# Performance work log

Hardware: AMD Instinct MI355X
Metric: run time of the kernel (lower is better)

Reference implementation:

```python
import jax, jax.numpy as jnp
import numpy as np

N, E, F, H, C = 100000, 1600000, 128, 128, 16
NEG_SLOPE = 0.01  # torch F.leaky_relu default


def setup_inputs() -> dict:
    key = jax.random.key(0)
    ks = jax.random.split(key, 32)
    inp = {
        "x": jax.random.normal(ks[0], (N, F), jnp.float32),
        "edge_index": jax.random.randint(ks[1], (2, E), 0, N, jnp.int32),
        "edge_weight": jax.random.uniform(ks[2], (E,), jnp.float32),
    }
    def w(k, fan_in, fan_out):
        s = 1.0 / np.sqrt(fan_in)
        return jax.random.uniform(k, (fan_in, fan_out), jnp.float32, -s, s)
    # cell 0: pre 128->128, arma 128->128, sage 128->128
    inp["pre_w0"] = w(ks[3], F, H); inp["pre_b0"] = jnp.zeros((H,), jnp.float32)
    inp["arma_w0"] = w(ks[4], H, H); inp["arma_v0"] = w(ks[5], H, H); inp["arma_b0"] = jnp.zeros((H,), jnp.float32)
    inp["sage_wl0"] = w(ks[6], H, H); inp["sage_bl0"] = jnp.zeros((H,), jnp.float32); inp["sage_wr0"] = w(ks[7], H, H)
    # cell 1: pre 256->128 (cell0 outputs 2H)
    inp["pre_w1"] = w(ks[8], 2 * H, H); inp["pre_b1"] = jnp.zeros((H,), jnp.float32)
    inp["arma_w1"] = w(ks[9], H, H); inp["arma_v1"] = w(ks[10], H, H); inp["arma_b1"] = jnp.zeros((H,), jnp.float32)
    inp["sage_wl1"] = w(ks[11], H, H); inp["sage_bl1"] = jnp.zeros((H,), jnp.float32); inp["sage_wr1"] = w(ks[12], H, H)
    inp["cls_w"] = w(ks[13], 2 * H, C); inp["cls_b"] = jnp.zeros((C,), jnp.float32)
    return inp


def _cell(h, row, col, norm, ew, cnt, n, arma_w, arma_v, arma_b, sage_wl, sage_bl, sage_wr):
    # ARMAConv (num_stacks=1, num_layers=1): relu(A_hat (h W) + h V + b), A_hat = sym-norm adj (no self loops)
    t = h @ arma_w
    agg = jax.ops.segment_sum(norm[:, None] * t[row], col, num_segments=n)
    h1 = jax.nn.leaky_relu(jax.nn.relu(agg + h @ arma_v + arma_b), NEG_SLOPE)
    # SAGEConv (mean aggr of edge-weighted messages): lin_l(mean_j w_ij h_j) + lin_r(h_i)
    s = jax.ops.segment_sum(ew[:, None] * h[row], col, num_segments=n)
    h2 = jax.nn.leaky_relu((s / cnt[:, None]) @ sage_wl + sage_bl + h @ sage_wr, NEG_SLOPE)
    return jax.nn.elu(jnp.concatenate([h1, h2], axis=1))


def reference(x, edge_index, edge_weight,
              pre_w0, pre_b0, arma_w0, arma_v0, arma_b0, sage_wl0, sage_bl0, sage_wr0,
              pre_w1, pre_b1, arma_w1, arma_v1, arma_b1, sage_wl1, sage_bl1, sage_wr1,
              cls_w, cls_b):
    n = x.shape[0]
    row, col = edge_index[0], edge_index[1]  # messages flow row -> col
    # gcn_norm without self loops (ARMAConv)
    deg = jax.ops.segment_sum(edge_weight, col, num_segments=n)
    dinv = jnp.where(deg > 0, 1.0 / jnp.sqrt(jnp.where(deg > 0, deg, 1.0)), 0.0)
    norm = dinv[row] * edge_weight * dinv[col]
    # scatter_mean denominator (edge counts, clamped to 1)
    cnt = jnp.maximum(jax.ops.segment_sum(jnp.ones_like(edge_weight), col, num_segments=n), 1.0)
    h = x  # eval mode: input dropout is identity
    for p in [(pre_w0, pre_b0, arma_w0, arma_v0, arma_b0, sage_wl0, sage_bl0, sage_wr0),
              (pre_w1, pre_b1, arma_w1, arma_v1, arma_b1, sage_wl1, sage_bl1, sage_wr1)]:
        pw, pb = p[0], p[1]
        h = _cell(h @ pw + pb, row, col, norm, edge_weight, cnt, n, *p[2:])
    logits = h @ cls_w + cls_b
    return jax.nn.log_softmax(logits, axis=-1)
```

## Files before the change

kernel.cpp:

```cpp
#include <hip/hip_runtime.h>
#include <hip/hip_bf16.h>
#include <hip/hip_fp16.h>

typedef __bf16 bf16x8 __attribute__((ext_vector_type(8)));
typedef float f32x4 __attribute__((ext_vector_type(4)));
typedef unsigned short ushort_t;
typedef unsigned int uint_t;

#if defined(__has_builtin)
#if __has_builtin(__builtin_amdgcn_global_load_lds)
#define HAS_GLL 1
#endif
#endif

__device__ inline float blo(uint_t v) { return __uint_as_float(v << 16); }
__device__ inline float bhi(uint_t v) { return __uint_as_float(v & 0xffff0000u); }
__device__ inline ushort_t f2b(float f) {
  uint_t u = __float_as_uint(f);
  uint_t r = (u + 0x7fffu + ((u >> 16) & 1u)) >> 16;
  return (ushort_t)r;
}
__device__ inline uint_t pk2(float a, float b) {
  return (uint_t)f2b(a) | ((uint_t)f2b(b) << 16);
}


__global__ __launch_bounds__(256) void bcount_k(const int* __restrict__ col,
                                                int* __restrict__ bcnt, int E, int NB) {
  __shared__ int h[256];
  int t = threadIdx.x;
  h[t] = 0;
  __syncthreads();
  int e0 = blockIdx.x * 8192;
#pragma unroll
  for (int j = 0; j < 32; ++j) {
    int e = e0 + j * 256 + t;
    if (e < E) atomicAdd(&h[col[e] >> 9], 1);
  }
  __syncthreads();
  if (t < NB && h[t] > 0) atomicAdd(&bcnt[t], h[t]);
}

__global__ __launch_bounds__(256) void bscan_k(const int* __restrict__ bcnt,
                                               int* __restrict__ bbase, int* __restrict__ cursor,
                                               int* __restrict__ offs, int NB, int N, int E) {
  __shared__ int sd[256];
  int t = threadIdx.x;
  int v = (t < NB) ? bcnt[t] : 0;
  int acc = v;
  sd[t] = v; __syncthreads();
  for (int off = 1; off < 256; off <<= 1) {
    int x = (t >= off) ? sd[t - off] : 0;
    __syncthreads();
    acc += x; sd[t] = acc;
    __syncthreads();
  }
  if (t < NB) { bbase[t] = acc - v; cursor[t] = acc - v; }
  if (t == 0) { bbase[NB] = E; offs[N] = E; }
}

__global__ __launch_bounds__(512) void bscatter_k(
    const int* __restrict__ row, const int* __restrict__ col, const float* __restrict__ ew,
    int* __restrict__ cursor, uint2* __restrict__ eout, int E, int NB) {
  __shared__ int h[256];
  __shared__ int lofs[256];
  __shared__ int lcur[256];
  __shared__ int gbase[256];
  __shared__ int sc[256];
  __shared__ uint2 stage[8192];
  __shared__ int addr[8192];
  int t = threadIdx.x;
  int e0 = blockIdx.x * 8192;
  int cnt = min(8192, E - e0);
  if (t < 256) h[t] = 0;
  __syncthreads();
#pragma unroll
  for (int j = 0; j < 16; ++j) {
    int e = e0 + j * 512 + t;
    if (e < E) atomicAdd(&h[col[e] >> 9], 1);
  }
  __syncthreads();
  int s = (t < 256) ? h[t] : 0;
  int acc = s;
  if (t < 256) sc[t] = s;
  __syncthreads();
  for (int off = 1; off < 256; off <<= 1) {
    int x = (t < 256 && t >= off) ? sc[t - off] : 0;
    __syncthreads();
    if (t < 256) { acc += x; sc[t] = acc; }
    __syncthreads();
  }
  if (t < NB && s > 0) gbase[t] = atomicAdd(&cursor[t], s);
  if (t < 256) { lofs[t] = acc - s; lcur[t] = acc - s; }
  __syncthreads();
#pragma unroll
  for (int j = 0; j < 16; ++j) {
    int e = e0 + j * 512 + t;
    if (e < E) {
      int c = col[e];
      int bk = c >> 9;
      int p = atomicAdd(&lcur[bk], 1);
      uint2 v;
      v.x = ((uint_t)(c & 511) << 17) | (uint_t)row[e];
      v.y = __float_as_uint(ew[e]);
      stage[p] = v;
      addr[p] = gbase[bk] + (p - lofs[bk]);
    }
  }
  __syncthreads();
  for (int i = t; i < cnt; i += 512) eout[addr[i]] = stage[i];
}

__global__ __launch_bounds__(512) void bsort_k(
    const uint2* __restrict__ ein, const int* __restrict__ bbase,
    int* __restrict__ offs, float* __restrict__ dinv, float* __restrict__ cinv,
    uint2* __restrict__ eout, int N) {
  __shared__ int h[512];
  __shared__ int lcur[512];
  __shared__ float degs[512];
  __shared__ int sd[512];
  int t = threadIdx.x, b = blockIdx.x;
  int base = bbase[b], end = bbase[b + 1];
  int cnt = end - base;
  int node0 = b << 9;
  h[t] = 0;
  degs[t] = 0.f;
  __syncthreads();
  for (int i = t; i < cnt; i += 512) {
    uint2 v = ein[base + i];
    int lc = v.x >> 17;
    atomicAdd(&h[lc], 1);
    atomicAdd(&degs[lc], __uint_as_float(v.y));
  }
  __syncthreads();
  int s = h[t];
  int acc = s;
  sd[t] = s; __syncthreads();
  for (int off = 1; off < 512; off <<= 1) {
    int x = (t >= off) ? sd[t - off] : 0;
    __syncthreads();
    acc += x; sd[t] = acc;
    __syncthreads();
  }
  int excl = acc - s;
  lcur[t] = excl;
  int node = node0 + t;
  if (node < N) {
    offs[node] = base + excl;
    float d = degs[t];
    dinv[node] = d > 0.f ? rsqrtf(d) : 0.f;
    cinv[node] = 1.0f / fmaxf((float)s, 1.f);
  }
  __syncthreads();
  for (int i = t; i < cnt; i += 512) {
    uint2 v = ein[base + i];
    int lc = v.x >> 17;
    int p = atomicAdd(&lcur[lc], 1);
    uint2 o;
    o.x = v.x & 0x1FFFF;
    o.y = v.y;
    eout[base + p] = o;
  }
}

__global__ void edgew_k(uint2* __restrict__ sedge, const float* __restrict__ dinv, int E) {
  int e = blockIdx.x * blockDim.x + threadIdx.x;
  if (e < E) {
    uint2 v = sedge[e];
    float ew = __uint_as_float(v.y);
    float wA = dinv[v.x] * ew;
    uint_t lo = (uint_t)__half_as_ushort(__float2half_rn(wA));
    uint_t hi = (uint_t)__half_as_ushort(__float2half_rn(ew));
    sedge[e].y = lo | (hi << 16);
  }
}

struct WP { const float* p[12]; };
__global__ void wtp_k(WP wp, ushort_t* __restrict__ wt) {
  int b = blockIdx.x;
  int t = threadIdx.x;
  if (b < 11) {
    const float* W = wp.p[b];
    ushort_t* T = wt + (size_t)b * 128 * 128;
    for (int i = 0; i < 64; ++i) {
      int lin = i * 256 + t;
      int k = lin >> 7, c = lin & 127;
      T[c * 128 + k] = f2b(W[lin]);
    }
  } else {
    const float* W = wp.p[11];
    ushort_t* T = wt + (size_t)11 * 128 * 128;
    for (int i = 0; i < 16; ++i) {
      int lin = i * 256 + t;
      int c = lin >> 8, k = lin & 255;
      T[lin] = f2b(W[k * 16 + c]);
    }
  }
}

__global__ __launch_bounds__(256) void agg_k(
    const uint_t* __restrict__ hp2, const uint2* __restrict__ sedge,
    const float* __restrict__ dinv, const float* __restrict__ cinv,
    const int* __restrict__ offs,
    uint_t* __restrict__ outA, uint_t* __restrict__ outS, int n) {
  int wid = threadIdx.x >> 6;
  int lane = threadIdx.x & 63;
  int half = lane >> 5, li = lane & 31;
  int node = blockIdx.x * 4 + wid;
  if (node >= n) return;
  int s0 = __builtin_amdgcn_readfirstlane(offs[node]);
  int e0 = __builtin_amdgcn_readfirstlane(offs[node + 1]);
  const char* hpb = (const char*)hp2;
  uint_t libase = (uint_t)(li << 3);
  float a0 = 0.f, a1 = 0.f, a2 = 0.f, a3 = 0.f;
  float m0 = 0.f, m1 = 0.f, m2 = 0.f, m3 = 0.f;
  for (int p = s0; p < e0; p += 8) {
    uint2 ed[4];
#pragma unroll
    for (int j = 0; j < 4; ++j) {
      int k = p + 2 * j + half;
      ed[j] = sedge[k < e0 ? k : s0];
    }
#pragma unroll
    for (int j = 0; j < 4; ++j) {
      int k = p + 2 * j + half;
      bool ok = (k < e0);
      uint_t w = ok ? ed[j].y : 0u;
      uint2 v = *(const uint2*)(hpb + ((ed[j].x << 8) | libase));
      float wA = __half2float(__ushort_as_half((ushort_t)(w & 0xffff)));
      float wS = __half2float(__ushort_as_half((ushort_t)(w >> 16)));
      float f0 = blo(v.x), f1 = bhi(v.x), f2 = blo(v.y), f3 = bhi(v.y);
      a0 += wA * f0; a1 += wA * f1; a2 += wA * f2; a3 += wA * f3;
      m0 += wS * f0; m1 += wS * f1; m2 += wS * f2; m3 += wS * f3;
    }
  }
  a0 += __shfl_xor(a0, 32); a1 += __shfl_xor(a1, 32);
  a2 += __shfl_xor(a2, 32); a3 += __shfl_xor(a3, 32);
  m0 += __shfl_xor(m0, 32); m1 += __shfl_xor(m1, 32);
  m2 += __shfl_xor(m2, 32); m3 += __shfl_xor(m3, 32);
  if (half == 0) {
    float dn = dinv[node];
    uint2 o;
    o.x = pk2(dn * a0, dn * a1);
    o.y = pk2(dn * a2, dn * a3);
    *(uint2*)&outA[(size_t)node * 64 + li * 2] = o;
  } else {
    float cn = cinv[node];
    uint2 o;
    o.x = pk2(cn * m0, cn * m1);
    o.y = pk2(cn * m2, cn * m3);
    *(uint2*)&outS[(size_t)node * 64 + li * 2] = o;
  }
}

__device__ inline int swz(int r, int k) { return (r * 128 + k) ^ ((r & 7) << 3); }
__device__ inline int cswz(int r, int k) { return (r * 256 + k) ^ ((r & 7) << 3); }

__device__ inline void stage_tile(const ushort_t* __restrict__ A, ushort_t* lds,
                                  int rowBase, int wid, int lane) {
  int lr = lane >> 4, lchunk = lane & 15;
#ifdef HAS_GLL
#pragma unroll
  for (int i = 0; i < 8; ++i) {
    int r = wid * 32 + i * 4 + lr;
    int csrc = (lchunk ^ (r & 7)) << 4;
    const char* g = (const char*)A + (((size_t)(rowBase + r)) << 8) + csrc;
    char* l = (char*)lds + ((wid * 32 + i * 4) << 8);
    __builtin_amdgcn_global_load_lds((const __attribute__((address_space(1))) void*)g,
                                     (__attribute__((address_space(3))) void*)l, 16, 0, 0);
  }
#else
#pragma unroll
  for (int i = 0; i < 8; ++i) {
    int r = wid * 32 + i * 4 + lr;
    uint4 v = *(const uint4*)&A[((size_t)(rowBase + r)) * 128 + lchunk * 8];
    *(uint4*)&lds[swz(r, lchunk * 8)] = v;
  }
#endif
}

__device__ inline void stage_wait() {
#ifdef HAS_GLL
  asm volatile("s_waitcnt vmcnt(0)" ::: "memory");
#endif
}

__device__ inline bf16x8 ldw(const ushort_t* __restrict__ Wt, int wc, int nn, int k, int lane) {
  int c = wc * 64 + nn * 16 + (lane & 15);
  return *(const bf16x8*)&Wt[c * 128 + k * 32 + (lane >> 4) * 8];
}

__device__ inline bf16x8 lda(const ushort_t* lds, int wr, int m, int k, int lane) {
  return *(const bf16x8*)&lds[swz(wr * 64 + m * 16 + (lane & 15), k * 32 + (lane >> 4) * 8)];
}

template <int ACT>
__device__ inline void epilogue(f32x4 (&acc)[4][4], const float* __restrict__ bias,
                                ushort_t* __restrict__ out, int rowBase, int wr, int wc,
                                int lane, int nrows) {
#pragma unroll
  for (int m = 0; m < 4; ++m) {
    int gr0 = rowBase + wr * 64 + m * 16 + (lane >> 4) * 4;
#pragma unroll
    for (int nn = 0; nn < 4; ++nn) {
      int gc = wc * 64 + nn * 16 + (lane & 15);
      float bv = bias[gc];
#pragma unroll
      for (int j = 0; j < 4; ++j) {
        int gr = gr0 + j;
        if (gr < nrows) {
          float v = acc[m][nn][j] + bv;
          if (ACT == 1) v = fmaxf(v, 0.f);
          if (ACT == 2) v = v > 0.f ? v : (__expf(0.01f * v) - 1.f);
          out[(size_t)gr * 128 + gc] = f2b(v);
        }
      }
    }
  }
}

__global__ __launch_bounds__(256, 2) void pre0_k(
    const float* __restrict__ Xf, const ushort_t* __restrict__ Wt,
    const float* __restrict__ bias, ushort_t* __restrict__ out, int nrows) {
  __shared__ ushort_t As[128 * 128];
  int t = threadIdx.x, lane = t & 63, wid = t >> 6;
  int wr = wid >> 1, wc = wid & 1;
  int rowBase = blockIdx.x * 128;
#pragma unroll
  for (int i = 0; i < 16; ++i) {
    int f = t + i * 256;
    int r = f >> 5, q = f & 31;
    int gr = rowBase + r;
    float4 v = make_float4(0.f, 0.f, 0.f, 0.f);
    if (gr < nrows) v = *(const float4*)&Xf[(size_t)gr * 128 + q * 4];
    uint2 o;
    o.x = pk2(v.x, v.y);
    o.y = pk2(v.z, v.w);
    *(uint2*)&As[swz(r, q * 4)] = o;
  }
  __syncthreads();
  f32x4 acc[4][4] = {};
#pragma unroll
  for (int k = 0; k < 4; ++k) {
    bf16x8 af[4], wf[4];
#pragma unroll
    for (int m = 0; m < 4; ++m) af[m] = lda(As, wr, m, k, lane);
#pragma unroll
    for (int nn = 0; nn < 4; ++nn) wf[nn] = ldw(Wt, wc, nn, k, lane);
#pragma unroll
    for (int m = 0; m < 4; ++m)
#pragma unroll
      for (int nn = 0; nn < 4; ++nn)
        acc[m][nn] = __builtin_amdgcn_mfma_f32_16x16x32_bf16(af[m], wf[nn], acc[m][nn], 0, 0, 0);
  }
  epilogue<0>(acc, bias, out, rowBase, wr, wc, lane, nrows);
}

template <int TAIL>
__global__ __launch_bounds__(256, 2) void dualfused_k(
    const ushort_t* __restrict__ X, const ushort_t* __restrict__ Y,
    const ushort_t* __restrict__ H,
    const ushort_t* __restrict__ WX, const ushort_t* __restrict__ WXH,
    const ushort_t* __restrict__ WY, const ushort_t* __restrict__ WYH,
    const float* __restrict__ bX, const float* __restrict__ bY,
    const ushort_t* __restrict__ WZ1, const ushort_t* __restrict__ WZ2,
    const float* __restrict__ bZ,
    ushort_t* __restrict__ outH, float* __restrict__ outL, int nrows) {
  __shared__ ushort_t buf[2 * 128 * 128];
  ushort_t* Xs = buf;
  ushort_t* Hs = buf + 128 * 128;
  int t = threadIdx.x, lane = t & 63, wid = t >> 6;
  int wr = wid >> 1, wc = wid & 1;
  int rowBase = blockIdx.x * 128;

  stage_tile(X, Xs, rowBase, wid, lane);
  stage_tile(H, Hs, rowBase, wid, lane);
  stage_wait();
  __syncthreads();

  uint_t h1p[4][4][2];
  {
    f32x4 acc[4][4] = {};
#pragma unroll
    for (int k = 0; k < 4; ++k) {
      bf16x8 af[4], hf[4], wx[4], wh[4];
#pragma unroll
      for (int m = 0; m < 4; ++m) { af[m] = lda(Xs, wr, m, k, lane); hf[m] = lda(Hs, wr, m, k, lane); }
#pragma unroll
      for (int nn = 0; nn < 4; ++nn) { wx[nn] = ldw(WX, wc, nn, k, lane); wh[nn] = ldw(WXH, wc, nn, k, lane); }
#pragma unroll
      for (int m = 0; m < 4; ++m)
#pragma unroll
        for (int nn = 0; nn < 4; ++nn) {
          acc[m][nn] = __builtin_amdgcn_mfma_f32_16x16x32_bf16(af[m], wx[nn], acc[m][nn], 0, 0, 0);
          acc[m][nn] = __builtin_amdgcn_mfma_f32_16x16x32_bf16(hf[m], wh[nn], acc[m][nn], 0, 0, 0);
        }
    }
#pragma unroll
    for (int m = 0; m < 4; ++m)
#pragma unroll
      for (int nn = 0; nn < 4; ++nn) {
        float bv = bX[wc * 64 + nn * 16 + (lane & 15)];
        float v0 = fmaxf(acc[m][nn][0] + bv, 0.f);
        float v1 = fmaxf(acc[m][nn][1] + bv, 0.f);
        float v2 = fmaxf(acc[m][nn][2] + bv, 0.f);
        float v3 = fmaxf(acc[m][nn][3] + bv, 0.f);
        h1p[m][nn][0] = pk2(v0, v1);
        h1p[m][nn][1] = pk2(v2, v3);
      }
  }

  __syncthreads();
  stage_tile(Y, Xs, rowBase, wid, lane);
  stage_wait();
  __syncthreads();

  f32x4 acc2[4][4] = {};
#pragma unroll
  for (int k = 0; k < 4; ++k) {
    bf16x8 af[4], hf[4], wy[4], wh[4];
#pragma unroll
    for (int m = 0; m < 4; ++m) { af[m] = lda(Xs, wr, m, k, lane); hf[m] = lda(Hs, wr, m, k, lane); }
#pragma unroll
    for (int nn = 0; nn < 4; ++nn) { wy[nn] = ldw(WY, wc, nn, k, lane); wh[nn] = ldw(WYH, wc, nn, k, lane); }
#pragma unroll
    for (int m = 0; m < 4; ++m)
#pragma unroll
      for (int nn = 0; nn < 4; ++nn) {
        acc2[m][nn] = __builtin_amdgcn_mfma_f32_16x16x32_bf16(af[m], wy[nn], acc2[m][nn], 0, 0, 0);
        acc2[m][nn] = __builtin_amdgcn_mfma_f32_16x16x32_bf16(hf[m], wh[nn], acc2[m][nn], 0, 0, 0);
      }
  }

  __syncthreads();

#pragma unroll
  for (int m = 0; m < 4; ++m) {
    int r0 = wr * 64 + m * 16 + (lane >> 4) * 4;
#pragma unroll
    for (int nn = 0; nn < 4; ++nn) {
      int c = wc * 64 + nn * 16 + (lane & 15);
      float bv = bY[c];
#pragma unroll
      for (int j = 0; j < 4; ++j) {
        int r = r0 + j;
        ushort_t h1v = (ushort_t)((h1p[m][nn][j >> 1] >> ((j & 1) * 16)) & 0xffff);
        buf[cswz(r, c)] = h1v;
        float v = acc2[m][nn][j] + bv;
        v = v > 0.f ? v : (__expf(0.01f * v) - 1.f);
        buf[cswz(r, 128 + c)] = f2b(v);
      }
    }
  }
  __syncthreads();

  if (TAIL == 0) {
    f32x4 acc3[4][4] = {};
#pragma unroll
    for (int kk = 0; kk < 8; ++kk) {
      const ushort_t* WZ = (kk < 4) ? WZ1 : WZ2;
      int kl = kk & 3;
      bf16x8 af[4], wf[4];
#pragma unroll
      for (int m = 0; m < 4; ++m) {
        int r = wr * 64 + m * 16 + (lane & 15);
        af[m] = *(const bf16x8*)&buf[cswz(r, kk * 32 + (lane >> 4) * 8)];
      }
#pragma unroll
      for (int nn = 0; nn < 4; ++nn) wf[nn] = ldw(WZ, wc, nn, kl, lane);
#pragma unroll
      for (int m = 0; m < 4; ++m)
#pragma unroll
        for (int nn = 0; nn < 4; ++nn)
          acc3[m][nn] = __builtin_amdgcn_mfma_f32_16x16x32_bf16(af[m], wf[nn], acc3[m][nn], 0, 0, 0);
    }
    epilogue<0>(acc3, bZ, outH, rowBase, wr, wc, lane, nrows);
  } else {
    f32x4 accc[2] = {};
#pragma unroll
    for (int kk = 0; kk < 8; ++kk) {
      bf16x8 bfr = *(const bf16x8*)&WZ1[(lane & 15) * 256 + kk * 32 + (lane >> 4) * 8];
#pragma unroll
      for (int mm = 0; mm < 2; ++mm) {
        int r = wid * 32 + mm * 16 + (lane & 15);
        bf16x8 af = *(const bf16x8*)&buf[cswz(r, kk * 32 + (lane >> 4) * 8)];
        accc[mm] = __builtin_amdgcn_mfma_f32_16x16x32_bf16(af, bfr, accc[mm], 0, 0, 0);
      }
    }
    float bc = bZ[lane & 15];
#pragma unroll
    for (int mm = 0; mm < 2; ++mm) {
#pragma unroll
      for (int j = 0; j < 4; ++j) {
        float lg = accc[mm][j] + bc;
        float mx = lg;
        for (int d = 1; d < 16; d <<= 1) mx = fmaxf(mx, __shfl_xor(mx, d));
        float ex = __expf(lg - mx);
        float sum = ex;
        for (int d = 1; d < 16; d <<= 1) sum += __shfl_xor(sum, d);
        float r_ = (lg - mx) - logf(sum);
        int grow = rowBase + wid * 32 + mm * 16 + (lane >> 4) * 4 + j;
        if (grow < nrows) outL[grow * 16 + (lane & 15)] = r_;
      }
    }
  }
}


extern "C" void kernel_launch(void* const* d_in, const int* in_sizes, int n_in,
                              void* d_out, int out_size, void* d_ws, size_t ws_size,
                              hipStream_t stream) {
  const float* x        = (const float*)d_in[0];
  const int*   eidx     = (const int*)d_in[1];
  const float* ew       = (const float*)d_in[2];
  const float* pre_w0   = (const float*)d_in[3];
  const float* pre_b0   = (const float*)d_in[4];
  const float* arma_w0  = (const float*)d_in[5];
  const float* arma_v0  = (const float*)d_in[6];
  const float* arma_b0  = (const float*)d_in[7];
  const float* sage_wl0 = (const float*)d_in[8];
  const float* sage_bl0 = (const float*)d_in[9];
  const float* sage_wr0 = (const float*)d_in[10];
  const float* pre_w1   = (const float*)d_in[11];
  const float* pre_b1   = (const float*)d_in[12];
  const float* arma_w1  = (const float*)d_in[13];
  const float* arma_v1  = (const float*)d_in[14];
  const float* arma_b1  = (const float*)d_in[15];
  const float* sage_wl1 = (const float*)d_in[16];
  const float* sage_bl1 = (const float*)d_in[17];
  const float* sage_wr1 = (const float*)d_in[18];
  const float* cls_w    = (const float*)d_in[19];
  const float* cls_b    = (const float*)d_in[20];

  const int N = in_sizes[0] / 128;
  const int E = in_sizes[2];
  const int N_pad = ((N + 127) / 128) * 128;
  const int NB = (N + 511) >> 9;
  const int* row = eidx;
  const int* col = eidx + E;

  char* p = (char*)d_ws;
  auto carve = [&](size_t bytes) { char* q = p; p += (bytes + 255) & ~(size_t)255; return q; };
  ushort_t* hp    = (ushort_t*)carve((size_t)N_pad * 128 * 2);
  ushort_t* bufA  = (ushort_t*)carve((size_t)N_pad * 128 * 2);
  ushort_t* bufS  = (ushort_t*)carve((size_t)N_pad * 128 * 2);
  ushort_t* wt    = (ushort_t*)carve(((size_t)11 * 128 * 128 + 16 * 256) * 2);
  uint2*  sedge  = (uint2*)carve((size_t)E * 8);
  uint2*  sedgeT = (uint2*)carve((size_t)E * 8);
  float*  dinv  = (float*)carve((size_t)N * 4);
  float*  cinv  = (float*)carve((size_t)N * 4);
  int*    offs  = (int*)carve((size_t)(N + 1) * 4);
  int*    bcnt  = (int*)carve((size_t)256 * 4);
  int*    bbase = (int*)carve((size_t)257 * 4);
  int*    cursor= (int*)carve((size_t)256 * 4);

  hipMemsetAsync(bcnt, 0, (size_t)256 * 4, stream);

  const int gE = (E + 8191) / 8192;
  bcount_k<<<gE, 256, 0, stream>>>(col, bcnt, E, NB);
  bscan_k<<<1, 256, 0, stream>>>(bcnt, bbase, cursor, offs, NB, N, E);
  bscatter_k<<<gE, 512, 0, stream>>>(row, col, ew, cursor, sedgeT, E, NB);
  bsort_k<<<NB, 512, 0, stream>>>(sedgeT, bbase, offs, dinv, cinv, sedge, N);
  edgew_k<<<(E + 255) / 256, 256, 0, stream>>>(sedge, dinv, E);

  WP wp;
  wp.p[0] = pre_w0;  wp.p[1] = arma_w0; wp.p[2] = arma_v0;
  wp.p[3] = sage_wl0; wp.p[4] = sage_wr0;
  wp.p[5] = pre_w1;  wp.p[6] = pre_w1 + 128 * 128;
  wp.p[7] = arma_w1; wp.p[8] = arma_v1;
  wp.p[9] = sage_wl1; wp.p[10] = sage_wr1;
  wp.p[11] = cls_w;
  wtp_k<<<12, 256, 0, stream>>>(wp, wt);

  const int gB = (N + 127) / 128;
  const int gA = (N + 3) / 4;
  auto WT = [&](int i) { return wt + (size_t)i * 128 * 128; };

  pre0_k<<<gB, 256, 0, stream>>>(x, WT(0), pre_b0, hp, N);
  agg_k<<<gA, 256, 0, stream>>>((const uint_t*)hp, sedge, dinv, cinv, offs,
                                (uint_t*)bufA, (uint_t*)bufS, N);
  dualfused_k<0><<<gB, 256, 0, stream>>>(bufA, bufS, hp, WT(1), WT(2), WT(3), WT(4),
                                         arma_b0, sage_bl0, WT(5), WT(6), pre_b1,
                                         hp, nullptr, N);
  agg_k<<<gA, 256, 0, stream>>>((const uint_t*)hp, sedge, dinv, cinv, offs,
                                (uint_t*)bufA, (uint_t*)bufS, N);
  dualfused_k<1><<<gB, 256, 0, stream>>>(bufA, bufS, hp, WT(7), WT(8), WT(9), WT(10),
                                         arma_b1, sage_bl1, WT(11), nullptr, cls_b,
                                         nullptr, (float*)d_out, N);
}
```

Before: 371.1 us.

## Retile dual fused GEMM kernel to 64-row blocks and stage X/Y/H together

The dual fused kernel now handles 64 rows per block instead of 128, with each wave owning a 32-column slice. The X, Y and H tiles are staged into shared memory once, together, and both GEMM chains run in a single k-loop. This removes the second staging round and its barriers, cuts accumulator registers so launch bounds can allow three blocks per CU, and doubles the grid. In exchange each block loads the weights more often relative to the rows it computes, and the classifier tail now does one MFMA tile per wave.

Result: no change. 366.1 us (-1.4%).

```diff
diff --git a/kernel.cpp b/kernel.cpp
--- a/kernel.cpp
+++ b/kernel.cpp
@@ -256,6 +256,29 @@
 __device__ inline int swz(int r, int k) { return (r * 128 + k) ^ ((r & 7) << 3); }
 __device__ inline int cswz(int r, int k) { return (r * 256 + k) ^ ((r & 7) << 3); }
 
+__device__ inline void stage_tile64(const ushort_t* __restrict__ A, ushort_t* lds,
+                                    int rowBase, int wid, int lane) {
+  int lr = lane >> 4, lchunk = lane & 15;
+#ifdef HAS_GLL
+#pragma unroll
+  for (int i = 0; i < 4; ++i) {
+    int r = wid * 16 + i * 4 + lr;
+    int csrc = (lchunk ^ (r & 7)) << 4;
+    const char* g = (const char*)A + (((size_t)(rowBase + r)) << 8) + csrc;
+    char* l = (char*)lds + ((wid * 16 + i * 4) << 8);
+    __builtin_amdgcn_global_load_lds((const __attribute__((address_space(1))) void*)g,
+                                     (__attribute__((address_space(3))) void*)l, 16, 0, 0);
+  }
+#else
+#pragma unroll
+  for (int i = 0; i < 4; ++i) {
+    int r = wid * 16 + i * 4 + lr;
+    uint4 v = *(const uint4*)&A[((size_t)(rowBase + r)) * 128 + lchunk * 8];
+    *(uint4*)&lds[swz(r, lchunk * 8)] = v;
+  }
+#endif
+}
+
 __device__ inline void stage_tile(const ushort_t* __restrict__ A, ushort_t* lds,
                                   int rowBase, int wid, int lane) {
   int lr = lane >> 4, lchunk = lane & 15;
@@ -285,38 +308,12 @@
 #endif
 }
 
-__device__ inline bf16x8 ldw(const ushort_t* __restrict__ Wt, int wc, int nn, int k, int lane) {
-  int c = wc * 64 + nn * 16 + (lane & 15);
+__device__ inline bf16x8 ldw(const ushort_t* __restrict__ Wt, int c, int k, int lane) {
   return *(const bf16x8*)&Wt[c * 128 + k * 32 + (lane >> 4) * 8];
 }
 
-__device__ inline bf16x8 lda(const ushort_t* lds, int wr, int m, int k, int lane) {
-  return *(const bf16x8*)&lds[swz(wr * 64 + m * 16 + (lane & 15), k * 32 + (lane >> 4) * 8)];
-}
-
-template <int ACT>
-__device__ inline void epilogue(f32x4 (&acc)[4][4], const float* __restrict__ bias,
-                                ushort_t* __restrict__ out, int rowBase, int wr, int wc,
-                                int lane, int nrows) {
-#pragma unroll
-  for (int m = 0; m < 4; ++m) {
-    int gr0 = rowBase + wr * 64 + m * 16 + (lane >> 4) * 4;
-#pragma unroll
-    for (int nn = 0; nn < 4; ++nn) {
-      int gc = wc * 64 + nn * 16 + (lane & 15);
-      float bv = bias[gc];
-#pragma unroll
-      for (int j = 0; j < 4; ++j) {
-        int gr = gr0 + j;
-        if (gr < nrows) {
-          float v = acc[m][nn][j] + bv;
-          if (ACT == 1) v = fmaxf(v, 0.f);
-          if (ACT == 2) v = v > 0.f ? v : (__expf(0.01f * v) - 1.f);
-          out[(size_t)gr * 128 + gc] = f2b(v);
-        }
-      }
-    }
-  }
+__device__ inline bf16x8 lda64(const ushort_t* lds, int m, int k, int lane) {
+  return *(const bf16x8*)&lds[swz(m * 16 + (lane & 15), k * 32 + (lane >> 4) * 8)];
 }
 
 __global__ __launch_bounds__(256, 2) void pre0_k(
@@ -344,20 +341,34 @@
   for (int k = 0; k < 4; ++k) {
     bf16x8 af[4], wf[4];
 #pragma unroll
-    for (int m = 0; m < 4; ++m) af[m] = lda(As, wr, m, k, lane);
-#pragma unroll
-    for (int nn = 0; nn < 4; ++nn) wf[nn] = ldw(Wt, wc, nn, k, lane);
+    for (int m = 0; m < 4; ++m)
+      af[m] = *(const bf16x8*)&As[swz(wr * 64 + m * 16 + (lane & 15), k * 32 + (lane >> 4) * 8)];
+#pragma unroll
+    for (int nn = 0; nn < 4; ++nn) wf[nn] = ldw(Wt, wc * 64 + nn * 16 + (lane & 15), k, lane);
 #pragma unroll
     for (int m = 0; m < 4; ++m)
 #pragma unroll
       for (int nn = 0; nn < 4; ++nn)
         acc[m][nn] = __builtin_amdgcn_mfma_f32_16x16x32_bf16(af[m], wf[nn], acc[m][nn], 0, 0, 0);
   }
-  epilogue<0>(acc, bias, out, rowBase, wr, wc, lane, nrows);
+#pragma unroll
+  for (int m = 0; m < 4; ++m) {
+    int gr0 = rowBase + wr * 64 + m * 16 + (lane >> 4) * 4;
+#pragma unroll
+    for (int nn = 0; nn < 4; ++nn) {
+      int gc = wc * 64 + nn * 16 + (lane & 15);
+      float bv = bias[gc];
+#pragma unroll
+      for (int j = 0; j < 4; ++j) {
+        int gr = gr0 + j;
+        if (gr < nrows) out[(size_t)gr * 128 + gc] = f2b(acc[m][nn][j] + bv);
+      }
+    }
+  }
 }
 
 template <int TAIL>
-__global__ __launch_bounds__(256, 2) void dualfused_k(
+__global__ __launch_bounds__(256, 3) void dualfused_k(
     const ushort_t* __restrict__ X, const ushort_t* __restrict__ Y,
     const ushort_t* __restrict__ H,
     const ushort_t* __restrict__ WX, const ushort_t* __restrict__ WXH,
@@ -366,142 +377,125 @@
     const ushort_t* __restrict__ WZ1, const ushort_t* __restrict__ WZ2,
     const float* __restrict__ bZ,
     ushort_t* __restrict__ outH, float* __restrict__ outL, int nrows) {
-  __shared__ ushort_t buf[2 * 128 * 128];
+  __shared__ ushort_t buf[3 * 64 * 128];
   ushort_t* Xs = buf;
-  ushort_t* Hs = buf + 128 * 128;
+  ushort_t* Ys = buf + 64 * 128;
+  ushort_t* Hs = buf + 2 * 64 * 128;
   int t = threadIdx.x, lane = t & 63, wid = t >> 6;
-  int wr = wid >> 1, wc = wid & 1;
-  int rowBase = blockIdx.x * 128;
-
-  stage_tile(X, Xs, rowBase, wid, lane);
-  stage_tile(H, Hs, rowBase, wid, lane);
+  int rowBase = blockIdx.x * 64;
+  int c16 = lane & 15;
+
+  stage_tile64(X, Xs, rowBase, wid, lane);
+  stage_tile64(Y, Ys, rowBase, wid, lane);
+  stage_tile64(H, Hs, rowBase, wid, lane);
   stage_wait();
   __syncthreads();
 
-  uint_t h1p[4][4][2];
-  {
-    f32x4 acc[4][4] = {};
-#pragma unroll
-    for (int k = 0; k < 4; ++k) {
-      bf16x8 af[4], hf[4], wx[4], wh[4];
-#pragma unroll
-      for (int m = 0; m < 4; ++m) { af[m] = lda(Xs, wr, m, k, lane); hf[m] = lda(Hs, wr, m, k, lane); }
-#pragma unroll
-      for (int nn = 0; nn < 4; ++nn) { wx[nn] = ldw(WX, wc, nn, k, lane); wh[nn] = ldw(WXH, wc, nn, k, lane); }
-#pragma unroll
-      for (int m = 0; m < 4; ++m)
-#pragma unroll
-        for (int nn = 0; nn < 4; ++nn) {
-          acc[m][nn] = __builtin_amdgcn_mfma_f32_16x16x32_bf16(af[m], wx[nn], acc[m][nn], 0, 0, 0);
-          acc[m][nn] = __builtin_amdgcn_mfma_f32_16x16x32_bf16(hf[m], wh[nn], acc[m][nn], 0, 0, 0);
-        }
+  f32x4 acc1[4][2] = {};
+  f32x4 acc2[4][2] = {};
+#pragma unroll
+  for (int k = 0; k < 4; ++k) {
+    bf16x8 xf[4], yf[4], hf[4], wx[2], whx[2], wy[2], why[2];
+#pragma unroll
+    for (int m = 0; m < 4; ++m) {
+      xf[m] = lda64(Xs, m, k, lane);
+      yf[m] = lda64(Ys, m, k, lane);
+      hf[m] = lda64(Hs, m, k, lane);
+    }
+#pragma unroll
+    for (int nn = 0; nn < 2; ++nn) {
+      int c = wid * 32 + nn * 16 + c16;
+      wx[nn] = ldw(WX, c, k, lane);
+      whx[nn] = ldw(WXH, c, k, lane);
+      wy[nn] = ldw(WY, c, k, lane);
+      why[nn] = ldw(WYH, c, k, lane);
     }
 #pragma unroll
     for (int m = 0; m < 4; ++m)
 #pragma unroll
-      for (int nn = 0; nn < 4; ++nn) {
-        float bv = bX[wc * 64 + nn * 16 + (lane & 15)];
-        float v0 = fmaxf(acc[m][nn][0] + bv, 0.f);
-        float v1 = fmaxf(acc[m][nn][1] + bv, 0.f);
-        float v2 = fmaxf(acc[m][nn][2] + bv, 0.f);
-        float v3 = fmaxf(acc[m][nn][3] + bv, 0.f);
-        h1p[m][nn][0] = pk2(v0, v1);
-        h1p[m][nn][1] = pk2(v2, v3);
+      for (int nn = 0; nn < 2; ++nn) {
+        acc1[m][nn] = __builtin_amdgcn_mfma_f32_16x16x32_bf16(xf[m], wx[nn], acc1[m][nn], 0, 0, 0);
+        acc1[m][nn] = __builtin_amdgcn_mfma_f32_16x16x32_bf16(hf[m], whx[nn], acc1[m][nn], 0, 0, 0);
+        acc2[m][nn] = __builtin_amdgcn_mfma_f32_16x16x32_bf16(yf[m], wy[nn], acc2[m][nn], 0, 0, 0);
+        acc2[m][nn] = __builtin_amdgcn_mfma_f32_16x16x32_bf16(hf[m], why[nn], acc2[m][nn], 0, 0, 0);
       }
   }
 
   __syncthreads();
-  stage_tile(Y, Xs, rowBase, wid, lane);
-  stage_wait();
-  __syncthreads();
-
-  f32x4 acc2[4][4] = {};
-#pragma unroll
-  for (int k = 0; k < 4; ++k) {
-    bf16x8 af[4], hf[4], wy[4], wh[4];
-#pragma unroll
-    for (int m = 0; m < 4; ++m) { af[m] = lda(Xs, wr, m, k, lane); hf[m] = lda(Hs, wr, m, k, lane); }
-#pragma unroll
-    for (int nn = 0; nn < 4; ++nn) { wy[nn] = ldw(WY, wc, nn, k, lane); wh[nn] = ldw(WYH, wc, nn, k, lane); }
-#pragma unroll
-    for (int m = 0; m < 4; ++m)
-#pragma unroll
-      for (int nn = 0; nn < 4; ++nn) {
-        acc2[m][nn] = __builtin_amdgcn_mfma_f32_16x16x32_bf16(af[m], wy[nn], acc2[m][nn], 0, 0, 0);
-        acc2[m][nn] = __builtin_amdgcn_mfma_f32_16x16x32_bf16(hf[m], wh[nn], acc2[m][nn], 0, 0, 0);
-      }
-  }
-
-  __syncthreads();
 
 #pragma unroll
   for (int m = 0; m < 4; ++m) {
-    int r0 = wr * 64 + m * 16 + (lane >> 4) * 4;
-#pragma unroll
-    for (int nn = 0; nn < 4; ++nn) {
-      int c = wc * 64 + nn * 16 + (lane & 15);
-      float bv = bY[c];
+    int r0 = m * 16 + (lane >> 4) * 4;
+#pragma unroll
+    for (int nn = 0; nn < 2; ++nn) {
+      int c = wid * 32 + nn * 16 + c16;
+      float bv1 = bX[c];
+      float bv2 = bY[c];
 #pragma unroll
       for (int j = 0; j < 4; ++j) {
         int r = r0 + j;
-        ushort_t h1v = (ushort_t)((h1p[m][nn][j >> 1] >> ((j & 1) * 16)) & 0xffff);
-        buf[cswz(r, c)] = h1v;
-        float v = acc2[m][nn][j] + bv;
-        v = v > 0.f ? v : (__expf(0.01f * v) - 1.f);
-        buf[cswz(r, 128 + c)] = f2b(v);
+        float v1 = fmaxf(acc1[m][nn][j] + bv1, 0.f);
+        buf[cswz(r, c)] = f2b(v1);
+        float v2 = acc2[m][nn][j] + bv2;
+        v2 = v2 > 0.f ? v2 : (__expf(0.01f * v2) - 1.f);
+        buf[cswz(r, 128 + c)] = f2b(v2);
       }
     }
   }
   __syncthreads();
 
   if (TAIL == 0) {
-    f32x4 acc3[4][4] = {};
+    f32x4 acc3[4][2] = {};
 #pragma unroll
     for (int kk = 0; kk < 8; ++kk) {
       const ushort_t* WZ = (kk < 4) ? WZ1 : WZ2;
       int kl = kk & 3;
-      bf16x8 af[4], wf[4];
-#pragma unroll
-      for (int m = 0; m < 4; ++m) {
-        int r = wr * 64 + m * 16 + (lane & 15);
-        af[m] = *(const bf16x8*)&buf[cswz(r, kk * 32 + (lane >> 4) * 8)];
+      bf16x8 af[4], wf[2];
+#pragma unroll
+      for (int m = 0; m < 4; ++m)
+        af[m] = *(const bf16x8*)&buf[cswz(m * 16 + c16, kk * 32 + (lane >> 4) * 8)];
+#pragma unroll
+      for (int nn = 0; nn < 2; ++nn) wf[nn] = ldw(WZ, wid * 32 + nn * 16 + c16, kl, lane);
+#pragma unroll
+      for (int m = 0; m < 4; ++m)
+#pragma unroll
+        for (int nn = 0; nn < 2; ++nn)
+          acc3[m][nn] = __builtin_amdgcn_mfma_f32_16x16x32_bf16(af[m], wf[nn], acc3[m][nn], 0, 0, 0);
+    }
+#pragma unroll
+    for (int m = 0; m < 4; ++m) {
+      int gr0 = rowBase + m * 16 + (lane >> 4) * 4;
+#pragma unroll
+      for (int nn = 0; nn < 2; ++nn) {
+        int gc = wid * 32 + nn * 16 + c16;
+        float bv = bZ[gc];
+#pragma unroll
+        for (int j = 0; j < 4; ++j) {
+          int gr = gr0 + j;
+          if (gr < nrows) outH[(size_t)gr * 128 + gc] = f2b(acc3[m][nn][j] + bv);
+        }
       }
-#pragma unroll
-      for (int nn = 0; nn < 4; ++nn) wf[nn] = ldw(WZ, wc, nn, kl, lane);
-#pragma unroll
-      for (int m = 0; m < 4; ++m)
-#pragma unroll
-        for (int nn = 0; nn < 4; ++nn)
-          acc3[m][nn] = __builtin_amdgcn_mfma_f32_16x16x32_bf16(af[m], wf[nn], acc3[m][nn], 0, 0, 0);
-    }
-    epilogue<0>(acc3, bZ, outH, rowBase, wr, wc, lane, nrows);
+    }
   } else {
-    f32x4 accc[2] = {};
+    f32x4 accc = {};
 #pragma unroll
     for (int kk = 0; kk < 8; ++kk) {
-      bf16x8 bfr = *(const bf16x8*)&WZ1[(lane & 15) * 256 + kk * 32 + (lane >> 4) * 8];
-#pragma unroll
-      for (int mm = 0; mm < 2; ++mm) {
-        int r = wid * 32 + mm * 16 + (lane & 15);
-        bf16x8 af = *(const bf16x8*)&buf[cswz(r, kk * 32 + (lane >> 4) * 8)];
-        accc[mm] = __builtin_amdgcn_mfma_f32_16x16x32_bf16(af, bfr, accc[mm], 0, 0, 0);
-      }
-    }
-    float bc = bZ[lane & 15];
-#pragma unroll
-    for (int mm = 0; mm < 2; ++mm) {
-#pragma unroll
-      for (int j = 0; j < 4; ++j) {
-        float lg = accc[mm][j] + bc;
-        float mx = lg;
-        for (int d = 1; d < 16; d <<= 1) mx = fmaxf(mx, __shfl_xor(mx, d));
-        float ex = __expf(lg - mx);
-        float sum = ex;
-        for (int d = 1; d < 16; d <<= 1) sum += __shfl_xor(sum, d);
-        float r_ = (lg - mx) - logf(sum);
-        int grow = rowBase + wid * 32 + mm * 16 + (lane >> 4) * 4 + j;
-        if (grow < nrows) outL[grow * 16 + (lane & 15)] = r_;
-      }
+      bf16x8 bfr = *(const bf16x8*)&WZ1[c16 * 256 + kk * 32 + (lane >> 4) * 8];
+      bf16x8 af = *(const bf16x8*)&buf[cswz(wid * 16 + c16, kk * 32 + (lane >> 4) * 8)];
+      accc = __builtin_amdgcn_mfma_f32_16x16x32_bf16(af, bfr, accc, 0, 0, 0);
+    }
+    float bc = bZ[c16];
+#pragma unroll
+    for (int j = 0; j < 4; ++j) {
+      float lg = accc[j] + bc;
+      float mx = lg;
+      for (int d = 1; d < 16; d <<= 1) mx = fmaxf(mx, __shfl_xor(mx, d));
+      float ex = __expf(lg - mx);
+      float sum = ex;
+      for (int d = 1; d < 16; d <<= 1) sum += __shfl_xor(sum, d);
+      float r_ = (lg - mx) - logf(sum);
+      int grow = rowBase + wid * 16 + (lane >> 4) * 4 + j;
+      if (grow < nrows) outL[grow * 16 + c16] = r_;
     }
   }
 }
@@ -573,18 +567,19 @@
   wtp_k<<<12, 256, 0, stream>>>(wp, wt);
 
   const int gB = (N + 127) / 128;
+  const int gB64 = (N + 63) / 64;
   const int gA = (N + 3) / 4;
   auto WT = [&](int i) { return wt + (size_t)i * 128 * 128; };
 
   pre0_k<<<gB, 256, 0, stream>>>(x, WT(0), pre_b0, hp, N);
   agg_k<<<gA, 256, 0, stream>>>((const uint_t*)hp, sedge, dinv, cinv, offs,
                                 (uint_t*)bufA, (uint_t*)bufS, N);
-  dualfused_k<0><<<gB, 256, 0, stream>>>(bufA, bufS, hp, WT(1), WT(2), WT(3), WT(4),
-                                         arma_b0, sage_bl0, WT(5), WT(6), pre_b1,
-                                         hp, nullptr, N);
+  dualfused_k<0><<<gB64, 256, 0, stream>>>(bufA, bufS, hp, WT(1), WT(2), WT(3), WT(4),
+                                           arma_b0, sage_bl0, WT(5), WT(6), pre_b1,
+                                           hp, nullptr, N);
   agg_k<<<gA, 256, 0, stream>>>((const uint_t*)hp, sedge, dinv, cinv, offs,
                                 (uint_t*)bufA, (uint_t*)bufS, N);
-  dualfused_k<1><<<gB, 256, 0, stream>>>(bufA, bufS, hp, WT(7), WT(8), WT(9), WT(10),
-                                         arma_b1, sage_bl1, WT(11), nullptr, cls_b,
-                                         nullptr, (float*)d_out, N);
-}
+  dualfused_k<1><<<gB64, 256, 0, stream>>>(bufA, bufS, hp, WT(7), WT(8), WT(9), WT(10),
+                                           arma_b1, sage_bl1, WT(11), nullptr, cls_b,
+                                           nullptr, (float*)d_out, N);
+}
```
